# Kernel optimization log

Measured on AMD Instinct MI355X. Metric: run time of the kernel, lower is better.

## Reference

```python
import jax, jax.numpy as jnp
import numpy as np

B, K, D, S, E = 256, 512, 64, 100000, 20000  # batch, knowledge_n, low_dim, student_n, exer_n


def setup_inputs() -> dict:
    key = jax.random.key(0)
    ks = jax.random.split(key, 10)
    stu_id = jax.random.randint(ks[0], (B,), 0, S)
    exer_id = jax.random.randint(ks[1], (B,), 0, E)
    kn_emb = jax.random.uniform(ks[2], (B, K), dtype=jnp.float32)
    # learned parameters (xavier-ish scale)
    stu_table = jax.random.normal(ks[3], (S, D), dtype=jnp.float32) * 0.05
    exer_table = jax.random.normal(ks[4], (E, D), dtype=jnp.float32) * 0.05
    kn_table = jax.random.normal(ks[5], (K, D), dtype=jnp.float32) * 0.05
    W1 = jax.random.normal(ks[6], (K, K + D), dtype=jnp.float32) * (2.0 / (2 * K + D)) ** 0.5
    W2 = jax.random.normal(ks[7], (K, K + D), dtype=jnp.float32) * (2.0 / (2 * K + D)) ** 0.5
    W3 = jax.random.normal(ks[8], (1, K), dtype=jnp.float32) * (2.0 / (K + 1)) ** 0.5
    b3 = jnp.zeros((1,), dtype=jnp.float32)
    return {"stu_id": stu_id, "exer_id": exer_id, "kn_emb": kn_emb,
            "stu_table": stu_table, "exer_table": exer_table, "kn_table": kn_table,
            "W1": W1, "W2": W2, "W3": W3, "b3": b3}


def reference(stu_id, exer_id, kn_emb, stu_table, exer_table, kn_table, W1, W2, W3, b3):
    k = kn_table.shape[0]  # knowledge_n
    # sigmoid(stu_emb @ kn_table.T): (B, K) per-concept proficiency / difficulty
    stu = jax.nn.sigmoid(stu_table[stu_id] @ kn_table.T)
    exer = jax.nn.sigmoid(exer_table[exer_id] @ kn_table.T)
    # Linear on cat([repeated stu/exer vec, kn_vector]) decomposes: split W into
    # the first K columns (acting on the batch vector, constant over the K axis)
    # and the last D columns (acting on kn_table, constant over batch).
    pref = jax.nn.sigmoid((stu @ W1[:, :k].T)[:, None, :] + (kn_table @ W1[:, k:].T)[None, :, :])  # (B,K,K)
    diff = jax.nn.sigmoid((exer @ W2[:, :k].T)[:, None, :] + (kn_table @ W2[:, k:].T)[None, :, :])  # (B,K,K)
    o = jax.nn.sigmoid(jnp.einsum('bkn,n->bk', pref - diff, W3[0]) + b3)  # (B,K)
    sum_out = jnp.sum(o * kn_emb, axis=1, keepdims=True)  # (B,1)
    count = jnp.sum(kn_emb, axis=1, keepdims=True)
    return sum_out / count
```

## Files before the change

### kernel.cpp

```cpp
#include <hip/hip_runtime.h>

#define B_ 256
#define K_ 512
#define D_ 64
#define KD_ 576
#define LOG2E 1.44269504088896340736f

typedef float v2f __attribute__((ext_vector_type(2)));
typedef float v4f __attribute__((ext_vector_type(4)));
typedef short bf16x8 __attribute__((ext_vector_type(8)));
typedef float f32x16 __attribute__((ext_vector_type(16)));

#define ZERO16 {0.f,0.f,0.f,0.f,0.f,0.f,0.f,0.f,0.f,0.f,0.f,0.f,0.f,0.f,0.f,0.f}

__device__ __forceinline__ float fexp2(float x) {
#if __has_builtin(__builtin_amdgcn_exp2f)
    return __builtin_amdgcn_exp2f(x);
#else
    float r; asm("v_exp_f32 %0, %1" : "=v"(r) : "v"(x)); return r;
#endif
}
__device__ __forceinline__ float frcp(float x) {
#if __has_builtin(__builtin_amdgcn_rcpf)
    return __builtin_amdgcn_rcpf(x);
#else
    float r; asm("v_rcp_f32 %0, %1" : "=v"(r) : "v"(x)); return r;
#endif
}
__device__ __forceinline__ float fsig(float x) {
    return frcp(1.0f + fexp2(-LOG2E * x));
}
__device__ __forceinline__ ushort f2bf(float f) {
    union { float f; unsigned u; } v; v.f = f;
    return (ushort)((v.u + 0x7FFFu + ((v.u >> 16) & 1u)) >> 16);
}
__device__ __forceinline__ bf16x8 ldcvt8(const float* p) {
    float4 a = *(const float4*)p;
    float4 b = *(const float4*)(p + 4);
    bf16x8 r;
    r[0] = (short)f2bf(a.x); r[1] = (short)f2bf(a.y);
    r[2] = (short)f2bf(a.z); r[3] = (short)f2bf(a.w);
    r[4] = (short)f2bf(b.x); r[5] = (short)f2bf(b.y);
    r[6] = (short)f2bf(b.z); r[7] = (short)f2bf(b.w);
    return r;
}

__global__ void __launch_bounds__(256) kPrep(const int* __restrict__ sid,
                                             const int* __restrict__ eid,
                                             const float* __restrict__ stu_t,
                                             const float* __restrict__ exer_t,
                                             const float* __restrict__ kn_t,
                                             const float* __restrict__ W1,
                                             const float* __restrict__ W2,
                                             ushort* __restrict__ Sbu,
                                             float* __restrict__ FT1,
                                             float* __restrict__ FT2) {
    __shared__ float fts[64][65];
    const int bid = blockIdx.x, t = threadIdx.x;
    const int l = t & 63, w = t >> 6;
    const int dk = (l >> 5) * 8;
    if (bid < 64) {
        const int tab = bid >> 5, bt = (bid >> 3) & 3, nt = bid & 7;
        const int b0 = bt * 64, n0 = nt * 64;
        const int brow = b0 + (w & 1) * 32 + (l & 31);
        const int ncol = n0 + (w >> 1) * 32 + (l & 31);
        const int id = (tab ? eid : sid)[brow];
        const float* ar = (tab ? exer_t : stu_t) + (size_t)id * D_;
        const float* br = kn_t + (size_t)ncol * D_;
        f32x16 acc = ZERO16;
#pragma unroll
        for (int kk = 0; kk < 4; kk++) {
            bf16x8 a = ldcvt8(ar + kk * 16 + dk);
            bf16x8 b = ldcvt8(br + kk * 16 + dk);
            acc = __builtin_amdgcn_mfma_f32_32x32x16_bf16(a, b, acc, 0, 0, 0);
        }
        ushort* So = Sbu + (size_t)tab * B_ * K_;
#pragma unroll
        for (int r = 0; r < 16; r++) {
            const int row = (r & 3) + 8 * (r >> 2) + 4 * (l >> 5);
            So[(size_t)(b0 + (w & 1) * 32 + row) * K_ + ncol] = f2bf(fsig(acc[r]));
        }
    } else {
        const int fid = bid - 64;
        const int mat = fid >> 6, kt = (fid >> 3) & 7, nt = fid & 7;
        const int k0 = kt * 64, n0 = nt * 64;
        const int krow = k0 + (w & 1) * 32 + (l & 31);
        const int ncol = n0 + (w >> 1) * 32 + (l & 31);
        const float* Wm = mat ? W2 : W1;
        const float* ar = kn_t + (size_t)krow * D_;
        const float* br = Wm + (size_t)ncol * KD_ + K_;
        f32x16 acc = ZERO16;
#pragma unroll
        for (int kk = 0; kk < 4; kk++) {
            bf16x8 a = ldcvt8(ar + kk * 16 + dk);
            bf16x8 b = ldcvt8(br + kk * 16 + dk);
            acc = __builtin_amdgcn_mfma_f32_32x32x16_bf16(a, b, acc, 0, 0, 0);
        }
        const int nl_ = (w >> 1) * 32 + (l & 31);
#pragma unroll
        for (int r = 0; r < 16; r++) {
            const int row = (r & 3) + 8 * (r >> 2) + 4 * (l >> 5);
            fts[nl_][(w & 1) * 32 + row] = fexp2(-LOG2E * acc[r]);
        }
        __syncthreads();
        float* Fo = mat ? FT2 : FT1;
#pragma unroll
        for (int i = 0; i < 16; i++) {
            const int q = i * 256 + t;
            const int r_ = q >> 6, c_ = q & 63;
            Fo[(size_t)(n0 + r_) * K_ + k0 + c_] = fts[r_][c_];
        }
    }
}

__global__ void __launch_bounds__(256) kE(const ushort* __restrict__ Sbu,
                                          const float* __restrict__ W1,
                                          const float* __restrict__ W2,
                                          float* __restrict__ E) {
    __shared__ float lacc[4][32][33];
    const int bid = blockIdx.x, t = threadIdx.x;
    const int nt = bid & 7, bt = (bid >> 3) & 7, mat = bid >> 6;
    const int l = t & 63, w = t >> 6;
    const int q = w & 1, h = w >> 1;
    const int m0 = nt * 64, b0 = bt * 32;
    const int arow = b0 + (l & 31);
    const int brow = m0 + q * 32 + (l & 31);
    const float* W = mat ? W2 : W1;
    const short* Sp = (const short*)Sbu + (size_t)(mat * B_ + arow) * K_
                      + h * 256 + (l >> 5) * 8;
    const float* Wp = W + (size_t)brow * KD_ + h * 256 + (l >> 5) * 8;
    f32x16 acc = ZERO16;
#pragma unroll
    for (int kk = 0; kk < 16; kk++) {
        bf16x8 a = *(const bf16x8*)(Sp + kk * 16);
        bf16x8 b = ldcvt8(Wp + kk * 16);
        acc = __builtin_amdgcn_mfma_f32_32x32x16_bf16(a, b, acc, 0, 0, 0);
    }
#pragma unroll
    for (int r = 0; r < 16; r++) {
        const int row = (r & 3) + 8 * (r >> 2) + 4 * (l >> 5);
        lacc[h * 2 + q][row][l & 31] = acc[r];
    }
    __syncthreads();
#pragma unroll
    for (int i = 0; i < 8; i++) {
        const int o = t + i * 256;
        const int q2 = o >> 10, row = (o >> 5) & 31, col = o & 31;
        const float v = lacc[q2][row][col] + lacc[2 + q2][row][col];
        E[(size_t)mat * B_ * K_ + (size_t)(b0 + row) * K_ + m0 + q2 * 32 + col]
            = fexp2(-LOG2E * v);
    }
}

__global__ void __launch_bounds__(512) kMain(const float* __restrict__ FT1,
                                             const float* __restrict__ FT2,
                                             const float* __restrict__ Ebase,
                                             const float* __restrict__ W3,
                                             const float* __restrict__ b3,
                                             const float* __restrict__ kn_emb,
                                             float* __restrict__ pO) {
    __shared__ float lds[8704];
    const int t = threadIdx.x;
    const int l = t & 63, w = t >> 6;
    const int kg = blockIdx.x, bg = blockIdx.y;
    const int b0 = bg * 8;
    const int k = kg * 64 + l;

#pragma unroll
    for (int c = 0; c < 2; c++) {
        const int combo = w * 2 + c;
        const int mat = combo >> 3, b = combo & 7;
        const float* src = Ebase + (size_t)mat * B_ * K_ + (size_t)(b0 + b) * K_;
#pragma unroll
        for (int j = 0; j < 8; j++) {
            const int n = j * 64 + l;
            lds[mat * 4096 + n * 8 + b] = src[n];
        }
    }
    lds[8192 + t] = W3[t];
    const float b3v = b3[0];
    __syncthreads();

    const int nbase = w * 64;
    const float* f1p = FT1 + (size_t)nbase * K_ + k;
    const float* f2p = FT2 + (size_t)nbase * K_ + k;

    v2f acc0 = {0.f, 0.f}, acc1 = {0.f, 0.f}, acc2 = {0.f, 0.f}, acc3 = {0.f, 0.f};

#pragma unroll 4
    for (int nl = 0; nl < 64; nl++) {
        const float f1 = f1p[(size_t)nl * K_];
        const float f2 = f2p[(size_t)nl * K_];
        const int n = nbase + nl;
        const float w3n = lds[8192 + n];
        const v4f e1a = *(const v4f*)&lds[n * 8];
        const v4f e1b = *(const v4f*)&lds[n * 8 + 4];
        const v4f e2a = *(const v4f*)&lds[4096 + n * 8];
        const v4f e2b = *(const v4f*)&lds[4096 + n * 8 + 4];
        {
            const v2f e1 = {e1a.x, e1a.y}, e2 = {e2a.x, e2a.y};
            const v2f pd = e1 * f1 + 1.0f, qd = e2 * f2 + 1.0f;
            const v2f den = pd * qd;
            v2f rc; rc.x = frcp(den.x); rc.y = frcp(den.y);
            acc0 += ((qd - pd) * w3n) * rc;
        }
        {
            const v2f e1 = {e1a.z, e1a.w}, e2 = {e2a.z, e2a.w};
            const v2f pd = e1 * f1 + 1.0f, qd = e2 * f2 + 1.0f;
            const v2f den = pd * qd;
            v2f rc; rc.x = frcp(den.x); rc.y = frcp(den.y);
            acc1 += ((qd - pd) * w3n) * rc;
        }
        {
            const v2f e1 = {e1b.x, e1b.y}, e2 = {e2b.x, e2b.y};
            const v2f pd = e1 * f1 + 1.0f, qd = e2 * f2 + 1.0f;
            const v2f den = pd * qd;
            v2f rc; rc.x = frcp(den.x); rc.y = frcp(den.y);
            acc2 += ((qd - pd) * w3n) * rc;
        }
        {
            const v2f e1 = {e1b.z, e1b.w}, e2 = {e2b.z, e2b.w};
            const v2f pd = e1 * f1 + 1.0f, qd = e2 * f2 + 1.0f;
            const v2f den = pd * qd;
            v2f rc; rc.x = frcp(den.x); rc.y = frcp(den.y);
            acc3 += ((qd - pd) * w3n) * rc;
        }
    }

    __syncthreads();
    {
        float* sa = lds + w * 512 + l * 8;
        *(v2f*)(sa + 0) = acc0;
        *(v2f*)(sa + 2) = acc1;
        *(v2f*)(sa + 4) = acc2;
        *(v2f*)(sa + 6) = acc3;
    }
    __syncthreads();
    float s = 0.f;
#pragma unroll
    for (int ww = 0; ww < 8; ww++) s += lds[ww * 512 + l * 8 + w];
    const float o = fsig(s + b3v);
    float g = o * kn_emb[(size_t)(b0 + w) * K_ + kg * 64 + l];
#pragma unroll
    for (int off = 32; off; off >>= 1) g += __shfl_xor(g, off, 64);
    if (l == 0) pO[bg * 64 + kg * 8 + w] = g;
}

__global__ void __launch_bounds__(512) kFin(const float* __restrict__ pO,
                                            const float* __restrict__ kn_emb,
                                            float* __restrict__ out) {
    const int t = threadIdx.x, l = t & 63, w = t >> 6;
    const int bg = blockIdx.x;
    const int b = bg * 8 + w;
    float den = 0.f;
#pragma unroll
    for (int c = 0; c < 8; c++) den += kn_emb[(size_t)b * K_ + c * 64 + l];
#pragma unroll
    for (int off = 32; off; off >>= 1) den += __shfl_xor(den, off, 64);
    float num = (l < 8) ? pO[bg * 64 + l * 8 + w] : 0.f;
    num += __shfl_xor(num, 1, 64);
    num += __shfl_xor(num, 2, 64);
    num += __shfl_xor(num, 4, 64);
    if (l == 0) out[b] = num / den;
}

extern "C" void kernel_launch(void* const* d_in, const int* in_sizes, int n_in,
                              void* d_out, int out_size, void* d_ws, size_t ws_size,
                              hipStream_t stream) {
    const int*   stu_id     = (const int*)d_in[0];
    const int*   exer_id    = (const int*)d_in[1];
    const float* kn_emb     = (const float*)d_in[2];
    const float* stu_table  = (const float*)d_in[3];
    const float* exer_table = (const float*)d_in[4];
    const float* kn_table   = (const float*)d_in[5];
    const float* W1         = (const float*)d_in[6];
    const float* W2         = (const float*)d_in[7];
    const float* W3         = (const float*)d_in[8];
    const float* b3         = (const float*)d_in[9];
    float* out = (float*)d_out;

    float* ws = (float*)d_ws;
    float* FT1      = ws;
    float* FT2      = FT1 + (size_t)K_ * K_;
    float* E        = FT2 + (size_t)K_ * K_;
    ushort* Sbu     = (ushort*)(E + 2 * (size_t)B_ * K_);
    float* pO       = (float*)(Sbu + 2 * (size_t)B_ * K_);

    kPrep<<<192, 256, 0, stream>>>(stu_id, exer_id, stu_table, exer_table,
                                   kn_table, W1, W2, Sbu, FT1, FT2);
    kE<<<128, 256, 0, stream>>>(Sbu, W1, W2, E);
    kMain<<<dim3(8, 32), 512, 0, stream>>>(FT1, FT2, E, W3, b3, kn_emb, pO);
    kFin<<<32, 512, 0, stream>>>(pO, kn_emb, out);
}
```

Measured before the change: 39.58 us.

## Split main reduction over n, rebalance prep kernels, move sigmoid into final kernel

Splits the inner n-reduction of the main kernel into two halves on a third grid dimension, doubling the block count and halving LDS per block. The non-linear sigmoid and kn_emb weighting move to the final kernel, which now reads full per-k partial sums. The FT computation moves from the first prep kernel into the E kernel so the student/exercise projection runs alone. The E GEMM is re-tiled into smaller 32x32 tiles with a 4-way K split. The cost is extra partial-sum traffic to global memory and a heavier final kernel.

Result: faster. 36.52 us (-7.7%).

```diff
diff --git a/kernel.cpp b/kernel.cpp
--- a/kernel.cpp
+++ b/kernel.cpp
@@ -45,28 +45,87 @@
     return r;
 }
 
-__global__ void __launch_bounds__(256) kPrep(const int* __restrict__ sid,
-                                             const int* __restrict__ eid,
-                                             const float* __restrict__ stu_t,
-                                             const float* __restrict__ exer_t,
-                                             const float* __restrict__ kn_t,
-                                             const float* __restrict__ W1,
-                                             const float* __restrict__ W2,
-                                             ushort* __restrict__ Sbu,
-                                             float* __restrict__ FT1,
-                                             float* __restrict__ FT2) {
-    __shared__ float fts[64][65];
+__global__ void __launch_bounds__(256) kS(const int* __restrict__ sid,
+                                          const int* __restrict__ eid,
+                                          const float* __restrict__ stu_t,
+                                          const float* __restrict__ exer_t,
+                                          const float* __restrict__ kn_t,
+                                          ushort* __restrict__ Sbu) {
     const int bid = blockIdx.x, t = threadIdx.x;
     const int l = t & 63, w = t >> 6;
     const int dk = (l >> 5) * 8;
-    if (bid < 64) {
-        const int tab = bid >> 5, bt = (bid >> 3) & 3, nt = bid & 7;
-        const int b0 = bt * 64, n0 = nt * 64;
-        const int brow = b0 + (w & 1) * 32 + (l & 31);
+    const int tab = bid >> 5, bt = (bid >> 3) & 3, nt = bid & 7;
+    const int b0 = bt * 64, n0 = nt * 64;
+    const int brow = b0 + (w & 1) * 32 + (l & 31);
+    const int ncol = n0 + (w >> 1) * 32 + (l & 31);
+    const int id = (tab ? eid : sid)[brow];
+    const float* ar = (tab ? exer_t : stu_t) + (size_t)id * D_;
+    const float* br = kn_t + (size_t)ncol * D_;
+    f32x16 acc = ZERO16;
+#pragma unroll
+    for (int kk = 0; kk < 4; kk++) {
+        bf16x8 a = ldcvt8(ar + kk * 16 + dk);
+        bf16x8 b = ldcvt8(br + kk * 16 + dk);
+        acc = __builtin_amdgcn_mfma_f32_32x32x16_bf16(a, b, acc, 0, 0, 0);
+    }
+    ushort* So = Sbu + (size_t)tab * B_ * K_;
+#pragma unroll
+    for (int r = 0; r < 16; r++) {
+        const int row = (r & 3) + 8 * (r >> 2) + 4 * (l >> 5);
+        So[(size_t)(b0 + (w & 1) * 32 + row) * K_ + ncol] = f2bf(fsig(acc[r]));
+    }
+}
+
+__global__ void __launch_bounds__(256) kEF(const ushort* __restrict__ Sbu,
+                                           const float* __restrict__ W1,
+                                           const float* __restrict__ W2,
+                                           const float* __restrict__ kn_t,
+                                           float* __restrict__ E,
+                                           float* __restrict__ FT1,
+                                           float* __restrict__ FT2) {
+    __shared__ float shm[4224];
+    const int bid = blockIdx.x, t = threadIdx.x;
+    const int l = t & 63, w = t >> 6;
+    if (bid < 256) {
+        const int mat = bid >> 7, bt = (bid >> 4) & 7, nt = bid & 15;
+        const int b0 = bt * 32, n0 = nt * 32;
+        const int arow = b0 + (l & 31);
+        const int nrow = n0 + (l & 31);
+        const int koff = w * 128 + (l >> 5) * 8;
+        const short* Sp = (const short*)Sbu + (size_t)(mat * B_ + arow) * K_ + koff;
+        const float* Wp = (mat ? W2 : W1) + (size_t)nrow * KD_ + koff;
+        f32x16 acc = ZERO16;
+#pragma unroll
+        for (int kk = 0; kk < 8; kk++) {
+            bf16x8 a = *(const bf16x8*)(Sp + kk * 16);
+            bf16x8 b = ldcvt8(Wp + kk * 16);
+            acc = __builtin_amdgcn_mfma_f32_32x32x16_bf16(a, b, acc, 0, 0, 0);
+        }
+#pragma unroll
+        for (int r = 0; r < 16; r++) {
+            const int row = (r & 3) + 8 * (r >> 2) + 4 * (l >> 5);
+            shm[w * 1056 + row * 33 + (l & 31)] = acc[r];
+        }
+        __syncthreads();
+#pragma unroll
+        for (int i = 0; i < 4; i++) {
+            const int o = i * 256 + t;
+            const int row = (o >> 5) & 31, col = o & 31;
+            const float v = shm[row * 33 + col] + shm[1056 + row * 33 + col]
+                          + shm[2112 + row * 33 + col] + shm[3168 + row * 33 + col];
+            E[(size_t)mat * B_ * K_ + (size_t)(b0 + row) * K_ + n0 + col]
+                = fexp2(-LOG2E * v);
+        }
+    } else {
+        const int fid = bid - 256;
+        const int mat = fid >> 6, kt = (fid >> 3) & 7, nt = fid & 7;
+        const int k0 = kt * 64, n0 = nt * 64;
+        const int krow = k0 + (w & 1) * 32 + (l & 31);
         const int ncol = n0 + (w >> 1) * 32 + (l & 31);
-        const int id = (tab ? eid : sid)[brow];
-        const float* ar = (tab ? exer_t : stu_t) + (size_t)id * D_;
-        const float* br = kn_t + (size_t)ncol * D_;
+        const int dk = (l >> 5) * 8;
+        const float* Wm = mat ? W2 : W1;
+        const float* ar = kn_t + (size_t)krow * D_;
+        const float* br = Wm + (size_t)ncol * KD_ + K_;
         f32x16 acc = ZERO16;
 #pragma unroll
         for (int kk = 0; kk < 4; kk++) {
@@ -74,33 +133,11 @@
             bf16x8 b = ldcvt8(br + kk * 16 + dk);
             acc = __builtin_amdgcn_mfma_f32_32x32x16_bf16(a, b, acc, 0, 0, 0);
         }
-        ushort* So = Sbu + (size_t)tab * B_ * K_;
+        const int nl_ = (w >> 1) * 32 + (l & 31);
 #pragma unroll
         for (int r = 0; r < 16; r++) {
             const int row = (r & 3) + 8 * (r >> 2) + 4 * (l >> 5);
-            So[(size_t)(b0 + (w & 1) * 32 + row) * K_ + ncol] = f2bf(fsig(acc[r]));
-        }
-    } else {
-        const int fid = bid - 64;
-        const int mat = fid >> 6, kt = (fid >> 3) & 7, nt = fid & 7;
-        const int k0 = kt * 64, n0 = nt * 64;
-        const int krow = k0 + (w & 1) * 32 + (l & 31);
-        const int ncol = n0 + (w >> 1) * 32 + (l & 31);
-        const float* Wm = mat ? W2 : W1;
-        const float* ar = kn_t + (size_t)krow * D_;
-        const float* br = Wm + (size_t)ncol * KD_ + K_;
-        f32x16 acc = ZERO16;
-#pragma unroll
-        for (int kk = 0; kk < 4; kk++) {
-            bf16x8 a = ldcvt8(ar + kk * 16 + dk);
-            bf16x8 b = ldcvt8(br + kk * 16 + dk);
-            acc = __builtin_amdgcn_mfma_f32_32x32x16_bf16(a, b, acc, 0, 0, 0);
-        }
-        const int nl_ = (w >> 1) * 32 + (l & 31);
-#pragma unroll
-        for (int r = 0; r < 16; r++) {
-            const int row = (r & 3) + 8 * (r >> 2) + 4 * (l >> 5);
-            fts[nl_][(w & 1) * 32 + row] = fexp2(-LOG2E * acc[r]);
+            shm[nl_ * 65 + (w & 1) * 32 + row] = fexp2(-LOG2E * acc[r]);
         }
         __syncthreads();
         float* Fo = mat ? FT2 : FT1;
@@ -108,47 +145,8 @@
         for (int i = 0; i < 16; i++) {
             const int q = i * 256 + t;
             const int r_ = q >> 6, c_ = q & 63;
-            Fo[(size_t)(n0 + r_) * K_ + k0 + c_] = fts[r_][c_];
-        }
-    }
-}
-
-__global__ void __launch_bounds__(256) kE(const ushort* __restrict__ Sbu,
-                                          const float* __restrict__ W1,
-                                          const float* __restrict__ W2,
-                                          float* __restrict__ E) {
-    __shared__ float lacc[4][32][33];
-    const int bid = blockIdx.x, t = threadIdx.x;
-    const int nt = bid & 7, bt = (bid >> 3) & 7, mat = bid >> 6;
-    const int l = t & 63, w = t >> 6;
-    const int q = w & 1, h = w >> 1;
-    const int m0 = nt * 64, b0 = bt * 32;
-    const int arow = b0 + (l & 31);
-    const int brow = m0 + q * 32 + (l & 31);
-    const float* W = mat ? W2 : W1;
-    const short* Sp = (const short*)Sbu + (size_t)(mat * B_ + arow) * K_
-                      + h * 256 + (l >> 5) * 8;
-    const float* Wp = W + (size_t)brow * KD_ + h * 256 + (l >> 5) * 8;
-    f32x16 acc = ZERO16;
-#pragma unroll
-    for (int kk = 0; kk < 16; kk++) {
-        bf16x8 a = *(const bf16x8*)(Sp + kk * 16);
-        bf16x8 b = ldcvt8(Wp + kk * 16);
-        acc = __builtin_amdgcn_mfma_f32_32x32x16_bf16(a, b, acc, 0, 0, 0);
-    }
-#pragma unroll
-    for (int r = 0; r < 16; r++) {
-        const int row = (r & 3) + 8 * (r >> 2) + 4 * (l >> 5);
-        lacc[h * 2 + q][row][l & 31] = acc[r];
-    }
-    __syncthreads();
-#pragma unroll
-    for (int i = 0; i < 8; i++) {
-        const int o = t + i * 256;
-        const int q2 = o >> 10, row = (o >> 5) & 31, col = o & 31;
-        const float v = lacc[q2][row][col] + lacc[2 + q2][row][col];
-        E[(size_t)mat * B_ * K_ + (size_t)(b0 + row) * K_ + m0 + q2 * 32 + col]
-            = fexp2(-LOG2E * v);
+            Fo[(size_t)(n0 + r_) * K_ + k0 + c_] = shm[r_ * 65 + c_];
+        }
     }
 }
 
@@ -156,13 +154,11 @@
                                              const float* __restrict__ FT2,
                                              const float* __restrict__ Ebase,
                                              const float* __restrict__ W3,
-                                             const float* __restrict__ b3,
-                                             const float* __restrict__ kn_emb,
-                                             float* __restrict__ pO) {
-    __shared__ float lds[8704];
+                                             float* __restrict__ pPart) {
+    __shared__ float lds[4352];
     const int t = threadIdx.x;
     const int l = t & 63, w = t >> 6;
-    const int kg = blockIdx.x, bg = blockIdx.y;
+    const int kg = blockIdx.x, bg = blockIdx.y, ns = blockIdx.z;
     const int b0 = bg * 8;
     const int k = kg * 64 + l;
 
@@ -170,33 +166,33 @@
     for (int c = 0; c < 2; c++) {
         const int combo = w * 2 + c;
         const int mat = combo >> 3, b = combo & 7;
-        const float* src = Ebase + (size_t)mat * B_ * K_ + (size_t)(b0 + b) * K_;
-#pragma unroll
-        for (int j = 0; j < 8; j++) {
-            const int n = j * 64 + l;
-            lds[mat * 4096 + n * 8 + b] = src[n];
-        }
-    }
-    lds[8192 + t] = W3[t];
-    const float b3v = b3[0];
+        const float* src = Ebase + (size_t)mat * B_ * K_ + (size_t)(b0 + b) * K_
+                         + ns * 256;
+#pragma unroll
+        for (int j = 0; j < 4; j++) {
+            const int nl = j * 64 + l;
+            lds[mat * 2048 + nl * 8 + b] = src[nl];
+        }
+    }
+    if (t < 256) lds[4096 + t] = W3[ns * 256 + t];
     __syncthreads();
 
-    const int nbase = w * 64;
-    const float* f1p = FT1 + (size_t)nbase * K_ + k;
-    const float* f2p = FT2 + (size_t)nbase * K_ + k;
+    const int nbase = w * 32;
+    const float* f1p = FT1 + (size_t)(ns * 256 + nbase) * K_ + k;
+    const float* f2p = FT2 + (size_t)(ns * 256 + nbase) * K_ + k;
 
     v2f acc0 = {0.f, 0.f}, acc1 = {0.f, 0.f}, acc2 = {0.f, 0.f}, acc3 = {0.f, 0.f};
 
 #pragma unroll 4
-    for (int nl = 0; nl < 64; nl++) {
+    for (int nl = 0; nl < 32; nl++) {
         const float f1 = f1p[(size_t)nl * K_];
         const float f2 = f2p[(size_t)nl * K_];
         const int n = nbase + nl;
-        const float w3n = lds[8192 + n];
+        const float w3n = lds[4096 + n];
         const v4f e1a = *(const v4f*)&lds[n * 8];
         const v4f e1b = *(const v4f*)&lds[n * 8 + 4];
-        const v4f e2a = *(const v4f*)&lds[4096 + n * 8];
-        const v4f e2b = *(const v4f*)&lds[4096 + n * 8 + 4];
+        const v4f e2a = *(const v4f*)&lds[2048 + n * 8];
+        const v4f e2b = *(const v4f*)&lds[2048 + n * 8 + 4];
         {
             const v2f e1 = {e1a.x, e1a.y}, e2 = {e2a.x, e2a.y};
             const v2f pd = e1 * f1 + 1.0f, qd = e2 * f2 + 1.0f;
@@ -239,28 +235,34 @@
     float s = 0.f;
 #pragma unroll
     for (int ww = 0; ww < 8; ww++) s += lds[ww * 512 + l * 8 + w];
-    const float o = fsig(s + b3v);
-    float g = o * kn_emb[(size_t)(b0 + w) * K_ + kg * 64 + l];
-#pragma unroll
-    for (int off = 32; off; off >>= 1) g += __shfl_xor(g, off, 64);
-    if (l == 0) pO[bg * 64 + kg * 8 + w] = g;
-}
-
-__global__ void __launch_bounds__(512) kFin(const float* __restrict__ pO,
+    pPart[(((size_t)ns * 32 + bg) * 8 + w) * K_ + kg * 64 + l] = s;
+}
+
+__global__ void __launch_bounds__(256) kFin(const float* __restrict__ pPart,
                                             const float* __restrict__ kn_emb,
+                                            const float* __restrict__ b3,
                                             float* __restrict__ out) {
     const int t = threadIdx.x, l = t & 63, w = t >> 6;
-    const int bg = blockIdx.x;
-    const int b = bg * 8 + w;
-    float den = 0.f;
-#pragma unroll
-    for (int c = 0; c < 8; c++) den += kn_emb[(size_t)b * K_ + c * 64 + l];
-#pragma unroll
-    for (int off = 32; off; off >>= 1) den += __shfl_xor(den, off, 64);
-    float num = (l < 8) ? pO[bg * 64 + l * 8 + w] : 0.f;
-    num += __shfl_xor(num, 1, 64);
-    num += __shfl_xor(num, 2, 64);
-    num += __shfl_xor(num, 4, 64);
+    const int b = blockIdx.x * 4 + w;
+    const int bg = b >> 3, bi = b & 7;
+    const float b3v = b3[0];
+    const float* p0 = pPart + (((size_t)0 * 32 + bg) * 8 + bi) * K_;
+    const float* p1 = pPart + (((size_t)1 * 32 + bg) * 8 + bi) * K_;
+    const float* ke = kn_emb + (size_t)b * K_;
+    float num = 0.f, den = 0.f;
+#pragma unroll
+    for (int c = 0; c < 8; c++) {
+        const int kk = c * 64 + l;
+        const float s = p0[kk] + p1[kk];
+        const float kv = ke[kk];
+        num = fmaf(fsig(s + b3v), kv, num);
+        den += kv;
+    }
+#pragma unroll
+    for (int off = 32; off; off >>= 1) {
+        num += __shfl_xor(num, off, 64);
+        den += __shfl_xor(den, off, 64);
+    }
     if (l == 0) out[b] = num / den;
 }
 
@@ -284,11 +286,11 @@
     float* FT2      = FT1 + (size_t)K_ * K_;
     float* E        = FT2 + (size_t)K_ * K_;
     ushort* Sbu     = (ushort*)(E + 2 * (size_t)B_ * K_);
-    float* pO       = (float*)(Sbu + 2 * (size_t)B_ * K_);
-
-    kPrep<<<192, 256, 0, stream>>>(stu_id, exer_id, stu_table, exer_table,
-                                   kn_table, W1, W2, Sbu, FT1, FT2);
-    kE<<<128, 256, 0, stream>>>(Sbu, W1, W2, E);
-    kMain<<<dim3(8, 32), 512, 0, stream>>>(FT1, FT2, E, W3, b3, kn_emb, pO);
-    kFin<<<32, 512, 0, stream>>>(pO, kn_emb, out);
-}
+    float* pPart    = (float*)(Sbu + 2 * (size_t)B_ * K_);
+
+    kS<<<64, 256, 0, stream>>>(stu_id, exer_id, stu_table, exer_table,
+                               kn_table, Sbu);
+    kEF<<<384, 256, 0, stream>>>(Sbu, W1, W2, kn_table, E, FT1, FT2);
+    kMain<<<dim3(8, 32, 2), 512, 0, stream>>>(FT1, FT2, E, W3, pPart);
+    kFin<<<64, 256, 0, stream>>>(pPart, kn_emb, b3, out);
+}
```
